# Kernel tuning notes

Measured on AMD Instinct MI355X. Metric: run time of the kernel, lower is better.

The kernel has to match this reference:

```python
import jax, jax.numpy as jnp
import numpy as np
import math

H = 8        # num_heads
D = 32       # dim_head
DEPTH = 1
LAMBDA_INIT = 0.8 - 0.6 * math.exp(-0.3 * DEPTH)
EPS = 1e-8


def setup_inputs() -> dict:
    key = jax.random.key(0)
    ks = jax.random.split(key, 9)
    B, T, IN_DIM, OUT_DIM = 2, 2048, 1024, 1024
    E = 2 * H * D  # 512
    inp = {
        "x": jax.random.normal(ks[0], (B, T, IN_DIM), dtype=jnp.float32),
        "Wq": jax.random.normal(ks[1], (IN_DIM, E), dtype=jnp.float32) * (IN_DIM ** -0.5),
        "Wkv": jax.random.normal(ks[2], (IN_DIM, 2 * E), dtype=jnp.float32) * (IN_DIM ** -0.5),
        "Wout": jax.random.normal(ks[3], (E, OUT_DIM), dtype=jnp.float32) * (E ** -0.5),
        "lambda_q1": 0.1 * jax.random.normal(ks[4], (D,), dtype=jnp.float32),
        "lambda_k1": 0.1 * jax.random.normal(ks[5], (D,), dtype=jnp.float32),
        "lambda_q2": 0.1 * jax.random.normal(ks[6], (D,), dtype=jnp.float32),
        "lambda_k2": 0.1 * jax.random.normal(ks[7], (D,), dtype=jnp.float32),
        "gamma": jnp.ones((2 * D,), dtype=jnp.float32),
    }
    return inp


def reference(x, Wq, Wkv, Wout, lambda_q1, lambda_k1, lambda_q2, lambda_k2, gamma):
    B, T, _ = x.shape
    scaling = D ** -0.5

    q = (x @ Wq).reshape(B, T, 2 * H, D).transpose(0, 2, 1, 3) * scaling  # [B,2H,T,D]
    kv = x @ Wkv
    k, v = jnp.split(kv, 2, axis=-1)
    k = k.reshape(B, T, 2 * H, D).transpose(0, 2, 1, 3)        # [B,2H,T,D]
    v = v.reshape(B, T, H, 2 * D).transpose(0, 2, 1, 3)        # [B,H,T,2D]

    dots = jnp.einsum('bhqd,bhkd->bhqk', q, k)                 # [B,2H,T,T]
    attn_w = jax.nn.softmax(dots.astype(jnp.float32), axis=-1).astype(dots.dtype)

    lam1 = jnp.exp(jnp.sum(lambda_q1 * lambda_k1))
    lam2 = jnp.exp(jnp.sum(lambda_q2 * lambda_k2))
    lam = lam1 - lam2 + LAMBDA_INIT

    attn_w = attn_w.reshape(B, H, 2, T, T)
    attn_w = attn_w[:, :, 0] - lam * attn_w[:, :, 1]           # [B,H,T,T]

    attn = jnp.einsum('bhqk,bhkd->bhqd', attn_w, v)            # [B,H,T,2D]

    rms = jnp.sqrt(jnp.mean(attn * attn, axis=-1, keepdims=True))
    attn = gamma * (attn / (rms + EPS))
    attn = attn * (1.0 - LAMBDA_INIT)

    attn = attn.transpose(0, 2, 1, 3).reshape(B, T, 2 * H * D)  # [B,T,E]
    return attn @ Wout
```

## Files before the change

### kernel.cpp

```cpp
#include <hip/hip_runtime.h>

typedef __attribute__((ext_vector_type(8)))  _Float16 half8;
typedef __attribute__((ext_vector_type(4)))  _Float16 half4;
typedef __attribute__((ext_vector_type(2)))  __fp16   fp16x2;
typedef __attribute__((ext_vector_type(4)))  float    f32x4;

#define MFMA16(a,b,c) __builtin_amdgcn_mfma_f32_16x16x32_f16(a,b,c,0,0,0)

#define QSCALE       0.17677669529663687f
#define LAMBDA_INIT  0.3555090675909693f
#define OUT_SCALE    0.6444909324090307f
#define LOG2E        1.4426950408889634f
#define MSHIFT       4.0f

#define EXP2(x) __builtin_amdgcn_exp2f(x)

__device__ __forceinline__ void gld16(const void* g, void* l) {
    __builtin_amdgcn_global_load_lds(
        (const __attribute__((address_space(1))) unsigned int*)g,
        (__attribute__((address_space(3))) unsigned int*)l, 16, 0, 0);
}

__device__ __forceinline__ void tr64(const float* __restrict__ src,
                                     _Float16* __restrict__ dst,
                                     int srcld, int dstld, int bx, int by) {
    __shared__ float t[64][65];
    int k0 = bx * 64, n0 = by * 64;
    int c = threadIdx.x & 63, rr = threadIdx.x >> 6;
#pragma unroll
    for (int ph = 0; ph < 16; ++ph) {
        int k = ph * 4 + rr;
        t[k][c] = src[(size_t)(k0 + k) * srcld + n0 + c];
    }
    __syncthreads();
#pragma unroll
    for (int ph = 0; ph < 16; ++ph) {
        int n = ph * 4 + rr;
        dst[(size_t)(n0 + n) * dstld + k0 + c] = (_Float16)t[c][n];
    }
}

__global__ __launch_bounds__(256) void k_prep(const float* __restrict__ x,
                                              const float* __restrict__ Wq,
                                              const float* __restrict__ Wkv,
                                              const float* __restrict__ Wout,
                                              _Float16* __restrict__ xh,
                                              _Float16* __restrict__ WallT,
                                              _Float16* __restrict__ WoutT) {
    int b = blockIdx.x;
    if (b < 4096) {
        int i = (b * 256 + threadIdx.x) * 4;
        f32x4 v = *(const f32x4*)(x + i);
        half4 h;
        h[0] = (_Float16)v[0]; h[1] = (_Float16)v[1];
        h[2] = (_Float16)v[2]; h[3] = (_Float16)v[3];
        *(half4*)(xh + i) = h;
    } else if (b < 4224) {
        int idx = b - 4096;
        tr64(Wq, WallT, 512, 1024, idx & 15, idx >> 4);
    } else if (b < 4480) {
        int idx = b - 4224;
        tr64(Wkv, WallT + 512 * 1024, 1024, 1024, idx & 15, idx >> 4);
    } else {
        int idx = b - 4480;
        tr64(Wout, WoutT, 1024, 512, idx & 7, idx >> 3);
    }
}

__device__ __forceinline__ void gemm_loop(const _Float16* __restrict__ A,
                                          const _Float16* __restrict__ Bt,
                                          int K, int bm, int bn,
                                          char* As, char* Bs,
                                          f32x4 (&acc)[4][4]) {
    int tid = threadIdx.x, lane = tid & 63, w = tid >> 6;
    int col16 = lane & 15, quad = lane >> 4;
    int wm = (w >> 1) << 6, wn = (w & 1) << 6;
    int r0 = tid >> 2;
    int kc = (tid & 3) << 3;
    const _Float16* ga0 = A  + (size_t)(bm + r0) * K + kc;
    const _Float16* ga1 = A  + (size_t)(bm + 64 + r0) * K + kc;
    const _Float16* gb0 = Bt + (size_t)(bn + r0) * K + kc;
    const _Float16* gb1 = Bt + (size_t)(bn + 64 + r0) * K + kc;
    char* lA = As + (w << 10);
    char* lB = Bs + (w << 10);

    gld16(ga0, lA);
    gld16(ga1, lA + 4096);
    gld16(gb0, lB);
    gld16(gb1, lB + 4096);

    for (int k0 = 0; k0 < K; k0 += 32) {
        __syncthreads();
        int cb = (k0 >> 5) & 1;
        if (k0 + 32 < K) {
            int nb = (cb ^ 1) << 13;
            gld16(ga0 + k0 + 32, lA + nb);
            gld16(ga1 + k0 + 32, lA + nb + 4096);
            gld16(gb0 + k0 + 32, lB + nb);
            gld16(gb1 + k0 + 32, lB + nb + 4096);
        }
        const char* Asc = As + (cb << 13);
        const char* Bsc = Bs + (cb << 13);
        half8 af[4], bf[4];
#pragma unroll
        for (int i = 0; i < 4; ++i)
            af[i] = *(const half8*)(Asc + ((wm + i * 16 + col16) << 6) + (quad << 4));
#pragma unroll
        for (int j = 0; j < 4; ++j)
            bf[j] = *(const half8*)(Bsc + ((wn + j * 16 + col16) << 6) + (quad << 4));
#pragma unroll
        for (int i = 0; i < 4; ++i)
#pragma unroll
            for (int j = 0; j < 4; ++j)
                acc[i][j] = MFMA16(af[i], bf[j], acc[i][j]);
    }
}

__global__ __launch_bounds__(256) void k_gemm_qkv(const _Float16* __restrict__ xh,
                                                  const _Float16* __restrict__ WallT,
                                                  _Float16* __restrict__ qbuf,
                                                  char* __restrict__ Kf,
                                                  char* __restrict__ Vf) {
    __shared__ __align__(16) char As[16384];
    __shared__ __align__(16) char Bs[16384];
    f32x4 acc[4][4] = {};
    int bm = blockIdx.x * 128, bn = blockIdx.y * 128;
    gemm_loop(xh, WallT, 1024, bm, bn, As, Bs, acc);

    int tid = threadIdx.x, lane = tid & 63, w = tid >> 6;
    int col16 = lane & 15, quad = lane >> 4;
    int wm = (w >> 1) << 6, wn = (w & 1) << 6;

    if (bn < 512) {
        const float s = QSCALE * LOG2E;
#pragma unroll
        for (int i = 0; i < 4; ++i)
#pragma unroll
            for (int j = 0; j < 4; ++j) {
                int n = bn + wn + j * 16 + col16;
                int m0 = bm + wm + i * 16 + quad * 4;
#pragma unroll
                for (int r = 0; r < 4; ++r)
                    qbuf[(size_t)(m0 + r) * 512 + n] = (_Float16)(acc[i][j][r] * s);
            }
    } else if (bn < 1024) {
#pragma unroll
        for (int j = 0; j < 4; ++j) {
            int n = bn + wn + j * 16 + col16 - 512;
            int pp = n >> 6, dd = n & 63, head = dd >> 5, d32 = dd & 31;
            int lbase = (d32 >> 3) << 4;
            int e2 = (d32 & 7) << 1;
            int fragb = head << 11;
#pragma unroll
            for (int i = 0; i < 4; ++i) {
                int m0 = bm + wm + i * 16 + quad * 4;
                int b = m0 >> 11, tok = m0 & 2047, kb = tok >> 5, kk = tok & 31;
                char* dst = Kf + (((size_t)((b * 8 + pp) * 64 + kb)) << 12)
                          + fragb + ((kk >> 4) << 10) + ((lbase + (kk & 15)) << 4) + e2;
#pragma unroll
                for (int r = 0; r < 4; ++r)
                    *(_Float16*)(dst + (r << 4)) = (_Float16)acc[i][j][r];
            }
        }
    } else {
#pragma unroll
        for (int j = 0; j < 4; ++j) {
            int n = bn + wn + j * 16 + col16 - 1024;
            int pp = n >> 6, ch = n & 63;
            int off_t = ((ch >> 4) << 10) + ((ch & 15) << 4);
#pragma unroll
            for (int i = 0; i < 4; ++i) {
                int m0 = bm + wm + i * 16 + quad * 4;
                int b = m0 >> 11, tok = m0 & 2047, kb = tok >> 5, kk = tok & 31;
                int quadv = (kk < 16) ? (kk >> 2) : ((kk - 16) >> 2);
                int e0 = (kk < 16) ? 0 : 4;
                half4 hv;
#pragma unroll
                for (int r = 0; r < 4; ++r) hv[r] = (_Float16)acc[i][j][r];
                *(half4*)(Vf + (((size_t)((b * 8 + pp) * 64 + kb)) << 12)
                          + off_t + (quadv << 8) + (e0 << 1)) = hv;
            }
        }
    }
}

__global__ __launch_bounds__(512, 4) void k_attn_fused(
        const _Float16* __restrict__ qbuf,
        const char* __restrict__ Kf,
        const char* __restrict__ Vf,
        const float* __restrict__ lq1,
        const float* __restrict__ lk1,
        const float* __restrict__ lq2,
        const float* __restrict__ lk2,
        const float* __restrict__ gamma,
        _Float16* __restrict__ attnO) {
    __shared__ __align__(16) char Sh[2][16384];
    __shared__ float Ls[2][8][16];

    int blk = blockIdx.x;
    int bp  = ((blk & 7) << 1) | ((blk >> 3) & 1);
    int r32 = blk >> 4;
    int p = bp & 7, bb = bp >> 3;
    int tid = threadIdx.x, lane = tid & 63, w = tid >> 6;
    int qt2 = w & 1, c = w >> 1;
    int col16 = lane & 15, quad = lane >> 4;

    int qrow = bb * 2048 + r32 * 32 + qt2 * 16 + col16;
    const _Float16* qb = qbuf + (size_t)qrow * 512 + p * 64;
    half8 q1 = *(const half8*)(qb + quad * 8);
    half8 q2 = *(const half8*)(qb + 32 + quad * 8);

    size_t bpoff = ((size_t)(bb * 8 + p)) << 18;
    int j0 = (tid >> 8) << 1;
    const char* ks = Kf + bpoff + ((size_t)j0 << 16) + ((tid & 255) << 4);
    int dko = (j0 << 12) + ((tid & 255) << 4);

    const char* vsrc = Vf + bpoff + ((size_t)c << 16) + (lane << 4);

    const f32x4 minit = {-MSHIFT, -MSHIFT, -MSHIFT, -MSHIFT};

    float l1 = 0.f, l2 = 0.f;
    f32x4 o1[4] = {}, o2[4] = {};

    gld16(ks, (char*)Sh + dko);
    gld16(ks + 65536, (char*)Sh + dko + 4096);

    for (int it = 0; it < 16; ++it) {
        __syncthreads();

        half8 vf0 = *(const half8*)(vsrc);
        half8 vf1 = *(const half8*)(vsrc + 1024);
        half8 vf2 = *(const half8*)(vsrc + 2048);
        half8 vf3 = *(const half8*)(vsrc + 3072);
        vsrc += 4096;

        if (it + 1 < 16) {
            char* d = (char*)Sh + (((it + 1) & 1) << 14) + dko;
            gld16(ks + ((size_t)(it + 1) << 12), d);
            gld16(ks + 65536 + ((size_t)(it + 1) << 12), d + 4096);
        }
        const char* kvb = (char*)Sh + ((it & 1) << 14) + (c << 12) + (lane << 4);

        half8 kf0 = *(const half8*)(kvb);
        half8 kf1 = *(const half8*)(kvb + 1024);
        half8 kf2 = *(const half8*)(kvb + 2048);
        half8 kf3 = *(const half8*)(kvb + 3072);
        f32x4 sa1 = MFMA16(kf0, q1, minit), sb1 = MFMA16(kf1, q1, minit);
        f32x4 sa2 = MFMA16(kf2, q2, minit), sb2 = MFMA16(kf3, q2, minit);

        union { half8 v; fp16x2 h[4]; } p1u, p2u;
        {
            float a0 = EXP2(sa1[0]), a1 = EXP2(sa1[1]);
            float a2 = EXP2(sa1[2]), a3 = EXP2(sa1[3]);
            float b0 = EXP2(sb1[0]), b1 = EXP2(sb1[1]);
            float b2 = EXP2(sb1[2]), b3 = EXP2(sb1[3]);
            l1 += ((a0 + a1) + (a2 + a3)) + ((b0 + b1) + (b2 + b3));
            p1u.h[0] = __builtin_amdgcn_cvt_pkrtz(a0, a1);
            p1u.h[1] = __builtin_amdgcn_cvt_pkrtz(a2, a3);
            p1u.h[2] = __builtin_amdgcn_cvt_pkrtz(b0, b1);
            p1u.h[3] = __builtin_amdgcn_cvt_pkrtz(b2, b3);
        }
        {
            float a0 = EXP2(sa2[0]), a1 = EXP2(sa2[1]);
            float a2 = EXP2(sa2[2]), a3 = EXP2(sa2[3]);
            float b0 = EXP2(sb2[0]), b1 = EXP2(sb2[1]);
            float b2 = EXP2(sb2[2]), b3 = EXP2(sb2[3]);
            l2 += ((a0 + a1) + (a2 + a3)) + ((b0 + b1) + (b2 + b3));
            p2u.h[0] = __builtin_amdgcn_cvt_pkrtz(a0, a1);
            p2u.h[1] = __builtin_amdgcn_cvt_pkrtz(a2, a3);
            p2u.h[2] = __builtin_amdgcn_cvt_pkrtz(b0, b1);
            p2u.h[3] = __builtin_amdgcn_cvt_pkrtz(b2, b3);
        }
        o1[0] = MFMA16(p1u.v, vf0, o1[0]); o2[0] = MFMA16(p2u.v, vf0, o2[0]);
        o1[1] = MFMA16(p1u.v, vf1, o1[1]); o2[1] = MFMA16(p2u.v, vf1, o2[1]);
        o1[2] = MFMA16(p1u.v, vf2, o1[2]); o2[2] = MFMA16(p2u.v, vf2, o2[2]);
        o1[3] = MFMA16(p1u.v, vf3, o1[3]); o2[3] = MFMA16(p2u.v, vf3, o2[3]);
    }

    l1 += __shfl_xor(l1, 16); l1 += __shfl_xor(l1, 32);
    l2 += __shfl_xor(l2, 16); l2 += __shfl_xor(l2, 32);

    __syncthreads();
    {
        _Float16* ob = (_Float16*)((char*)Sh + ((c * 2 + qt2) << 12)) + col16;
#pragma unroll
        for (int r = 0; r < 4; ++r) {
            _Float16* od = ob + (quad * 4 + r) * 128;
#pragma unroll
            for (int t = 0; t < 4; ++t) {
                od[t * 16]      = (_Float16)o1[t][r];
                od[64 + t * 16] = (_Float16)o2[t][r];
            }
        }
        if (quad == 0) { Ls[0][w][col16] = l1; Ls[1][w][col16] = l2; }
    }
    __syncthreads();

    int rr = tid >> 4, jj = tid & 15;
    int qrt = rr >> 4, r16 = rr & 15;
    float o1s[4] = {}, o2s[4] = {};
    float l1s = 0.f, l2s = 0.f;
#pragma unroll
    for (int cc = 0; cc < 4; ++cc) {
        const _Float16* ob = (const _Float16*)((char*)Sh + ((cc * 2 + qrt) << 12))
                           + r16 * 128 + jj * 4;
        half4 a  = *(const half4*)ob;
        half4 b2 = *(const half4*)(ob + 64);
#pragma unroll
        for (int e = 0; e < 4; ++e) { o1s[e] += (float)a[e]; o2s[e] += (float)b2[e]; }
        l1s += Ls[0][cc * 2 + qrt][r16];
        l2s += Ls[1][cc * 2 + qrt][r16];
    }
    float s1 = 0.f, s2 = 0.f;
#pragma unroll
    for (int i = 0; i < 32; ++i) { s1 += lq1[i] * lk1[i]; s2 += lq2[i] * lk2[i]; }
    float lam = __expf(s1) - __expf(s2) + LAMBDA_INIT;
    float il1 = 1.f / l1s, il2 = lam / l2s;
    float Of[4], ss = 0.f;
#pragma unroll
    for (int e = 0; e < 4; ++e) { Of[e] = o1s[e] * il1 - o2s[e] * il2; ss += Of[e] * Of[e]; }
    ss += __shfl_xor(ss, 1, 16); ss += __shfl_xor(ss, 2, 16);
    ss += __shfl_xor(ss, 4, 16); ss += __shfl_xor(ss, 8, 16);
    float rms = sqrtf(ss * 0.015625f);
    float sc = OUT_SCALE / (rms + 1e-8f);
    half4 o;
#pragma unroll
    for (int e = 0; e < 4; ++e) o[e] = (_Float16)(gamma[jj * 4 + e] * Of[e] * sc);
    *(half4*)(attnO + ((size_t)(bb * 2048 + r32 * 32 + rr) * 512) + p * 64 + jj * 4) = o;
}

__global__ __launch_bounds__(256) void k_gemm_out(const _Float16* __restrict__ attn,
                                                  const _Float16* __restrict__ WoutT,
                                                  float* __restrict__ out) {
    __shared__ __align__(16) char As[16384];
    __shared__ __align__(16) char Bs[16384];
    f32x4 acc[4][4] = {};
    int bm = blockIdx.x * 128, bn = blockIdx.y * 128;
    gemm_loop(attn, WoutT, 512, bm, bn, As, Bs, acc);

    int tid = threadIdx.x, lane = tid & 63, w = tid >> 6;
    int col16 = lane & 15, quad = lane >> 4;
    int wm = (w >> 1) << 6, wn = (w & 1) << 6;
#pragma unroll
    for (int i = 0; i < 4; ++i)
#pragma unroll
        for (int j = 0; j < 4; ++j) {
            int n = bn + wn + j * 16 + col16;
            int m0 = bm + wm + i * 16 + quad * 4;
#pragma unroll
            for (int r = 0; r < 4; ++r)
                out[(size_t)(m0 + r) * 1024 + n] = acc[i][j][r];
        }
}

extern "C" void kernel_launch(void* const* d_in, const int* in_sizes, int n_in,
                              void* d_out, int out_size, void* d_ws, size_t ws_size,
                              hipStream_t stream) {
    const float* x     = (const float*)d_in[0];
    const float* Wq    = (const float*)d_in[1];
    const float* Wkv   = (const float*)d_in[2];
    const float* Wout  = (const float*)d_in[3];
    const float* lq1   = (const float*)d_in[4];
    const float* lk1   = (const float*)d_in[5];
    const float* lq2   = (const float*)d_in[6];
    const float* lk2   = (const float*)d_in[7];
    const float* gamma = (const float*)d_in[8];
    float* out = (float*)d_out;

    char* ws = (char*)d_ws;
    _Float16* xh    = (_Float16*)(ws);
    _Float16* WallT = (_Float16*)(ws + 8388608);
    _Float16* WoutT = (_Float16*)(ws + 11534336);
    _Float16* qbuf  = (_Float16*)(ws + 12582912);
    char*     Kf    = (char*)(ws + 16777216);
    char*     Vf    = (char*)(ws + 20971520);
    _Float16* attn  = (_Float16*)(ws + 25165824);

    k_prep<<<4608, 256, 0, stream>>>(x, Wq, Wkv, Wout, xh, WallT, WoutT);
    k_gemm_qkv<<<dim3(32, 12), 256, 0, stream>>>(xh, WallT, qbuf, Kf, Vf);
    k_attn_fused<<<1024, 512, 0, stream>>>(qbuf, Kf, Vf, lq1, lk1, lq2, lk2, gamma, attn);
    k_gemm_out<<<dim3(32, 8), 256, 0, stream>>>(attn, WoutT, out);
}
```

Measured before the change: 164.8 us.

## Load K directly into registers with double buffering, dropping LDS staging and barriers

Replaces the shared-memory double-buffered K staging (global_load_lds plus a __syncthreads every iteration) with per-wave direct global loads into two register buffers, prefetching the next key block while computing the current one. The loop is unrolled by two to alternate the buffers. This removes the per-iteration block barriers and LDS round trips. In exchange, K is now fetched redundantly by waves that share a slice, and register pressure rises.

```diff
diff --git a/kernel.cpp b/kernel.cpp
--- a/kernel.cpp
+++ b/kernel.cpp
@@ -184,6 +184,49 @@
     }
 }
 
+#define ATTN_STEP(KC, KN, itv)                                                   \
+    {                                                                            \
+        int itb = (itv) << 12;                                                   \
+        int itn = (((itv) + 1) & 15) << 12;          \
+        half8 vf0 = *(const half8*)(vbase + itb);                                \
+        half8 vf1 = *(const half8*)(vbase + itb + 1024);                         \
+        half8 vf2 = *(const half8*)(vbase + itb + 2048);                         \
+        half8 vf3 = *(const half8*)(vbase + itb + 3072);                         \
+        KN[0] = *(const half8*)(kbase + itn);                                    \
+        KN[1] = *(const half8*)(kbase + itn + 1024);                             \
+        KN[2] = *(const half8*)(kbase + itn + 2048);                             \
+        KN[3] = *(const half8*)(kbase + itn + 3072);                             \
+        f32x4 sa1 = MFMA16(KC[0], q1, minit), sb1 = MFMA16(KC[1], q1, minit);    \
+        f32x4 sa2 = MFMA16(KC[2], q2, minit), sb2 = MFMA16(KC[3], q2, minit);    \
+        union { half8 v; fp16x2 h[4]; } p1u, p2u;                                \
+        {                                                                        \
+            float a0 = EXP2(sa1[0]), a1 = EXP2(sa1[1]);                          \
+            float a2 = EXP2(sa1[2]), a3 = EXP2(sa1[3]);                          \
+            float b0 = EXP2(sb1[0]), b1 = EXP2(sb1[1]);                          \
+            float b2 = EXP2(sb1[2]), b3 = EXP2(sb1[3]);                          \
+            l1 += ((a0 + a1) + (a2 + a3)) + ((b0 + b1) + (b2 + b3));             \
+            p1u.h[0] = __builtin_amdgcn_cvt_pkrtz(a0, a1);                       \
+            p1u.h[1] = __builtin_amdgcn_cvt_pkrtz(a2, a3);                       \
+            p1u.h[2] = __builtin_amdgcn_cvt_pkrtz(b0, b1);                       \
+            p1u.h[3] = __builtin_amdgcn_cvt_pkrtz(b2, b3);                       \
+        }                                                                        \
+        {                                                                        \
+            float a0 = EXP2(sa2[0]), a1 = EXP2(sa2[1]);                          \
+            float a2 = EXP2(sa2[2]), a3 = EXP2(sa2[3]);                          \
+            float b0 = EXP2(sb2[0]), b1 = EXP2(sb2[1]);                          \
+            float b2 = EXP2(sb2[2]), b3 = EXP2(sb2[3]);                          \
+            l2 += ((a0 + a1) + (a2 + a3)) + ((b0 + b1) + (b2 + b3));             \
+            p2u.h[0] = __builtin_amdgcn_cvt_pkrtz(a0, a1);                       \
+            p2u.h[1] = __builtin_amdgcn_cvt_pkrtz(a2, a3);                       \
+            p2u.h[2] = __builtin_amdgcn_cvt_pkrtz(b0, b1);                       \
+            p2u.h[3] = __builtin_amdgcn_cvt_pkrtz(b2, b3);                       \
+        }                                                                        \
+        o1[0] = MFMA16(p1u.v, vf0, o1[0]); o2[0] = MFMA16(p2u.v, vf0, o2[0]);    \
+        o1[1] = MFMA16(p1u.v, vf1, o1[1]); o2[1] = MFMA16(p2u.v, vf1, o2[1]);    \
+        o1[2] = MFMA16(p1u.v, vf2, o1[2]); o2[2] = MFMA16(p2u.v, vf2, o2[2]);    \
+        o1[3] = MFMA16(p1u.v, vf3, o1[3]); o2[3] = MFMA16(p2u.v, vf3, o2[3]);    \
+    }
+
 __global__ __launch_bounds__(512, 4) void k_attn_fused(
         const _Float16* __restrict__ qbuf,
         const char* __restrict__ Kf,
@@ -194,7 +237,7 @@
         const float* __restrict__ lk2,
         const float* __restrict__ gamma,
         _Float16* __restrict__ attnO) {
-    __shared__ __align__(16) char Sh[2][16384];
+    __shared__ __align__(16) char Sh[32768];
     __shared__ float Ls[2][8][16];
 
     int blk = blockIdx.x;
@@ -211,78 +254,30 @@
     half8 q2 = *(const half8*)(qb + 32 + quad * 8);
 
     size_t bpoff = ((size_t)(bb * 8 + p)) << 18;
-    int j0 = (tid >> 8) << 1;
-    const char* ks = Kf + bpoff + ((size_t)j0 << 16) + ((tid & 255) << 4);
-    int dko = (j0 << 12) + ((tid & 255) << 4);
-
-    const char* vsrc = Vf + bpoff + ((size_t)c << 16) + (lane << 4);
+    const char* kbase = Kf + bpoff + ((size_t)c << 16) + (lane << 4);
+    const char* vbase = Vf + bpoff + ((size_t)c << 16) + (lane << 4);
 
     const f32x4 minit = {-MSHIFT, -MSHIFT, -MSHIFT, -MSHIFT};
 
     float l1 = 0.f, l2 = 0.f;
     f32x4 o1[4] = {}, o2[4] = {};
 
-    gld16(ks, (char*)Sh + dko);
-    gld16(ks + 65536, (char*)Sh + dko + 4096);
-
-    for (int it = 0; it < 16; ++it) {
-        __syncthreads();
-
-        half8 vf0 = *(const half8*)(vsrc);
-        half8 vf1 = *(const half8*)(vsrc + 1024);
-        half8 vf2 = *(const half8*)(vsrc + 2048);
-        half8 vf3 = *(const half8*)(vsrc + 3072);
-        vsrc += 4096;
-
-        if (it + 1 < 16) {
-            char* d = (char*)Sh + (((it + 1) & 1) << 14) + dko;
-            gld16(ks + ((size_t)(it + 1) << 12), d);
-            gld16(ks + 65536 + ((size_t)(it + 1) << 12), d + 4096);
-        }
-        const char* kvb = (char*)Sh + ((it & 1) << 14) + (c << 12) + (lane << 4);
-
-        half8 kf0 = *(const half8*)(kvb);
-        half8 kf1 = *(const half8*)(kvb + 1024);
-        half8 kf2 = *(const half8*)(kvb + 2048);
-        half8 kf3 = *(const half8*)(kvb + 3072);
-        f32x4 sa1 = MFMA16(kf0, q1, minit), sb1 = MFMA16(kf1, q1, minit);
-        f32x4 sa2 = MFMA16(kf2, q2, minit), sb2 = MFMA16(kf3, q2, minit);
-
-        union { half8 v; fp16x2 h[4]; } p1u, p2u;
-        {
-            float a0 = EXP2(sa1[0]), a1 = EXP2(sa1[1]);
-            float a2 = EXP2(sa1[2]), a3 = EXP2(sa1[3]);
-            float b0 = EXP2(sb1[0]), b1 = EXP2(sb1[1]);
-            float b2 = EXP2(sb1[2]), b3 = EXP2(sb1[3]);
-            l1 += ((a0 + a1) + (a2 + a3)) + ((b0 + b1) + (b2 + b3));
-            p1u.h[0] = __builtin_amdgcn_cvt_pkrtz(a0, a1);
-            p1u.h[1] = __builtin_amdgcn_cvt_pkrtz(a2, a3);
-            p1u.h[2] = __builtin_amdgcn_cvt_pkrtz(b0, b1);
-            p1u.h[3] = __builtin_amdgcn_cvt_pkrtz(b2, b3);
-        }
-        {
-            float a0 = EXP2(sa2[0]), a1 = EXP2(sa2[1]);
-            float a2 = EXP2(sa2[2]), a3 = EXP2(sa2[3]);
-            float b0 = EXP2(sb2[0]), b1 = EXP2(sb2[1]);
-            float b2 = EXP2(sb2[2]), b3 = EXP2(sb2[3]);
-            l2 += ((a0 + a1) + (a2 + a3)) + ((b0 + b1) + (b2 + b3));
-            p2u.h[0] = __builtin_amdgcn_cvt_pkrtz(a0, a1);
-            p2u.h[1] = __builtin_amdgcn_cvt_pkrtz(a2, a3);
-            p2u.h[2] = __builtin_amdgcn_cvt_pkrtz(b0, b1);
-            p2u.h[3] = __builtin_amdgcn_cvt_pkrtz(b2, b3);
-        }
-        o1[0] = MFMA16(p1u.v, vf0, o1[0]); o2[0] = MFMA16(p2u.v, vf0, o2[0]);
-        o1[1] = MFMA16(p1u.v, vf1, o1[1]); o2[1] = MFMA16(p2u.v, vf1, o2[1]);
-        o1[2] = MFMA16(p1u.v, vf2, o1[2]); o2[2] = MFMA16(p2u.v, vf2, o2[2]);
-        o1[3] = MFMA16(p1u.v, vf3, o1[3]); o2[3] = MFMA16(p2u.v, vf3, o2[3]);
+    half8 krA[4], krB[4];
+    krA[0] = *(const half8*)(kbase);
+    krA[1] = *(const half8*)(kbase + 1024);
+    krA[2] = *(const half8*)(kbase + 2048);
+    krA[3] = *(const half8*)(kbase + 3072);
+
+    for (int it = 0; it < 16; it += 2) {
+        ATTN_STEP(krA, krB, it);
+        ATTN_STEP(krB, krA, it + 1);
     }
 
     l1 += __shfl_xor(l1, 16); l1 += __shfl_xor(l1, 32);
     l2 += __shfl_xor(l2, 16); l2 += __shfl_xor(l2, 32);
 
-    __syncthreads();
     {
-        _Float16* ob = (_Float16*)((char*)Sh + ((c * 2 + qt2) << 12)) + col16;
+        _Float16* ob = (_Float16*)(Sh + ((c * 2 + qt2) << 12)) + col16;
 #pragma unroll
         for (int r = 0; r < 4; ++r) {
             _Float16* od = ob + (quad * 4 + r) * 128;
@@ -302,7 +297,7 @@
     float l1s = 0.f, l2s = 0.f;
 #pragma unroll
     for (int cc = 0; cc < 4; ++cc) {
-        const _Float16* ob = (const _Float16*)((char*)Sh + ((cc * 2 + qrt) << 12))
+        const _Float16* ob = (const _Float16*)(Sh + ((cc * 2 + qrt) << 12))
                            + r16 * 128 + jj * 4;
         half4 a  = *(const half4*)ob;
         half4 b2 = *(const half4*)(ob + 64);
```

Result: slower. 173.3 us (+5.1%).
